# Performance work log

Hardware: AMD Instinct MI355X
Metric: run time of the kernel (lower is better)

## Reference

```python
import jax, jax.numpy as jnp
import numpy as np

D_MODEL = 1024
NUM_HEADS = 16
HEAD_DIM = D_MODEL // NUM_HEADS
SCALE = HEAD_DIM ** -0.5
BATCH = 4096
N_MODULES = 8


def setup_inputs() -> dict:
    key = jax.random.key(0)
    ks = jax.random.split(key, 7)
    s = 1.0 / np.sqrt(D_MODEL)
    return {
        "query": jax.random.normal(ks[0], (BATCH, D_MODEL), jnp.float32),
        "kv_stack": jax.random.normal(ks[1], (N_MODULES, BATCH, D_MODEL), jnp.float32),
        "Wq": jax.random.normal(ks[2], (D_MODEL, D_MODEL), jnp.float32) * s,
        "Wk": jax.random.normal(ks[3], (D_MODEL, D_MODEL), jnp.float32) * s,
        "Wv": jax.random.normal(ks[4], (D_MODEL, D_MODEL), jnp.float32) * s,
        "Wo": jax.random.normal(ks[5], (D_MODEL, D_MODEL), jnp.float32) * s,
        "bo": jnp.zeros((D_MODEL,), jnp.float32),
    }


def reference(query, kv_stack, Wq, Wk, Wv, Wo, bo):
    # query: [B, D]; kv_stack: [M, B, D] (stacked module representations)
    B = query.shape[0]
    M = kv_stack.shape[0]
    # projections (nn.Linear: x @ W.T), split into heads; seq_len == 1
    q = (query @ Wq.T).reshape(B, NUM_HEADS, HEAD_DIM)            # [B,H,hd]
    k = jnp.einsum("mbd,ed->mbe", kv_stack, Wk).reshape(M, B, NUM_HEADS, HEAD_DIM)
    v = jnp.einsum("mbd,ed->mbe", kv_stack, Wv).reshape(M, B, NUM_HEADS, HEAD_DIM)
    # scores over the single kv position: [M,B,H,1]
    scores = jnp.einsum("bhd,mbhd->mbh", q, k)[..., None] * SCALE
    attn_weights = jax.nn.softmax(scores, axis=-1)  # softmax over size-1 axis -> ones
    attn_output = attn_weights * v                   # [M,B,H,hd] (dropout is eval/no-op)
    attn_output = attn_output.reshape(M, B, D_MODEL)
    out = jnp.einsum("mbe,oe->mbo", attn_output, Wo) + bo + query  # residual per module
    return out  # [M, B, D] (stacked in kv order instead of the dict)
```

## Files before the change

kernel.cpp:

```cpp
#include <hip/hip_runtime.h>
#include <hip/hip_bf16.h>


typedef __attribute__((ext_vector_type(4))) float f32x4;
typedef __attribute__((ext_vector_type(8))) short short8;

#define D_MODEL 1024
#define BATCH   4096
#define M_ROWS  32768

__device__ __forceinline__ short f2bf(float f) {
    union { float f; unsigned u; } x; x.f = f;
    unsigned r = (x.u + 0x7fffu + ((x.u >> 16) & 1u)) >> 16;
    return (short)r;
}

__device__ __forceinline__ unsigned bfpk(float lo, float hi) {
    __hip_bfloat162 h = __float22bfloat162_rn(make_float2(lo, hi));
    unsigned u; __builtin_memcpy(&u, &h, 4); return u;
}

__device__ __forceinline__ short8 cvt8(float4 a, float4 b) {
    union { unsigned u[4]; short8 s; } r;
    r.u[0] = bfpk(a.x, a.y);
    r.u[1] = bfpk(a.z, a.w);
    r.u[2] = bfpk(b.x, b.y);
    r.u[3] = bfpk(b.z, b.w);
    return r.s;
}

__global__ __launch_bounds__(256) void fuse_w_kernel(
        const float* __restrict__ Wo, const float* __restrict__ Wv,
        short* __restrict__ Cw) {
    __shared__ __align__(16) short Ash[64][32];
    __shared__ __align__(16) short Bsh[64][32];
    const int t = threadIdx.x;
    const int lane = t & 63;
    const int w = t >> 6;
    const int wr = w >> 1, wc = w & 1;
    const int brow = blockIdx.y * 64;
    const int bcol = blockIdx.x * 64;

    f32x4 acc[2][2];
#pragma unroll
    for (int m = 0; m < 2; ++m)
#pragma unroll
        for (int n = 0; n < 2; ++n) acc[m][n] = (f32x4)(0.0f);

    for (int kt = 0; kt < 32; ++kt) {
        const float* ga = Wo + (size_t)(brow + (t >> 2)) * D_MODEL + kt * 32 + (t & 3) * 8;
        float4 a0 = *(const float4*)ga;
        float4 a1 = *(const float4*)(ga + 4);
        float4 bv[2];
#pragma unroll
        for (int j = 0; j < 2; ++j) {
            int lin = j * 256 + t;
            int e = lin >> 4, c4 = lin & 15;
            bv[j] = *(const float4*)(Wv + (size_t)(kt * 32 + e) * D_MODEL + bcol + c4 * 4);
        }
        *reinterpret_cast<short8*>(&Ash[t >> 2][(t & 3) * 8]) = cvt8(a0, a1);
#pragma unroll
        for (int j = 0; j < 2; ++j) {
            int lin = j * 256 + t;
            int e = lin >> 4, c4 = lin & 15;
            int d = c4 * 4;
            Bsh[d + 0][e] = f2bf(bv[j].x);
            Bsh[d + 1][e] = f2bf(bv[j].y);
            Bsh[d + 2][e] = f2bf(bv[j].z);
            Bsh[d + 3][e] = f2bf(bv[j].w);
        }
        __syncthreads();
        {
            const int r = lane & 15, q = lane >> 4;
            short8 af[2], bfr[2];
#pragma unroll
            for (int m = 0; m < 2; ++m)
                af[m] = *reinterpret_cast<const short8*>(&Ash[wr * 32 + m * 16 + r][q * 8]);
#pragma unroll
            for (int n = 0; n < 2; ++n)
                bfr[n] = *reinterpret_cast<const short8*>(&Bsh[wc * 32 + n * 16 + r][q * 8]);
#pragma unroll
            for (int m = 0; m < 2; ++m)
#pragma unroll
                for (int n = 0; n < 2; ++n)
                    acc[m][n] = __builtin_amdgcn_mfma_f32_16x16x32_bf16(
                        af[m], bfr[n], acc[m][n], 0, 0, 0);
        }
        __syncthreads();
    }

    const int r = lane & 15, q = lane >> 4;
#pragma unroll
    for (int m = 0; m < 2; ++m)
#pragma unroll
        for (int n = 0; n < 2; ++n)
#pragma unroll
            for (int j = 0; j < 4; ++j) {
                int o = brow + wr * 32 + m * 16 + q * 4 + j;
                int d = bcol + wc * 32 + n * 16 + r;
                Cw[(size_t)o * D_MODEL + d] = f2bf(acc[m][n][j]);
            }
}

struct AV { float4 v[2][2]; };

__global__ __launch_bounds__(256) void attn_gemm_kernel(
        const float* __restrict__ kv, const float* __restrict__ query,
        const short* __restrict__ Cw, const float* __restrict__ bo,
        float* __restrict__ out) {
    __shared__ __align__(16) short Ash[2][128][32];
    __shared__ __align__(16) short Bsh[2][128][32];
    const int t = threadIdx.x;
    const int lane = t & 63;
    const int w = t >> 6;
    const int wr = w >> 1, wc = w & 1;

    const int L = blockIdx.x;
    const int x = L & 7, j5 = L >> 3;
    const int bx = j5 & 7;
    const int rt = (j5 >> 3) * 8 + x;
    const int brow = rt * 128;

    f32x4 acc[4][4];
#pragma unroll
    for (int m = 0; m < 4; ++m)
#pragma unroll
        for (int n = 0; n < 4; ++n) acc[m][n] = (f32x4)(0.0f);

    auto load_a = [&](int kt) {
        AV a;
#pragma unroll
        for (int j = 0; j < 2; ++j) {
            const float* g = kv + (size_t)(brow + j * 64 + (t >> 2)) * D_MODEL
                             + kt * 32 + (t & 3) * 8;
            a.v[j][0] = *(const float4*)g;
            a.v[j][1] = *(const float4*)(g + 4);
        }
        return a;
    };
    auto stage_b = [&](int kt, int buf) {
#pragma unroll
        for (int i = 0; i < 2; ++i) {
            const short* g = Cw + (size_t)(bx * 128 + i * 64 + (t >> 2)) * D_MODEL
                             + kt * 32 + (t & 3) * 8;
            __builtin_amdgcn_global_load_lds(
                (const __attribute__((address_space(1))) void*)g,
                (__attribute__((address_space(3))) void*)
                    ((char*)&Bsh[buf][0][0] + i * 4096 + w * 1024),
                16, 0, 0);
        }
    };
    auto write_a = [&](int buf, const AV& a) {
#pragma unroll
        for (int j = 0; j < 2; ++j)
            *reinterpret_cast<short8*>(&Ash[buf][j * 64 + (t >> 2)][(t & 3) * 8]) =
                cvt8(a.v[j][0], a.v[j][1]);
    };
    auto compute = [&](int buf) {
        const int r = lane & 15, q = lane >> 4;
        short8 af[4], bfr[4];
#pragma unroll
        for (int m = 0; m < 4; ++m)
            af[m] = *reinterpret_cast<const short8*>(&Ash[buf][wr * 64 + m * 16 + r][q * 8]);
#pragma unroll
        for (int n = 0; n < 4; ++n)
            bfr[n] = *reinterpret_cast<const short8*>(&Bsh[buf][wc * 64 + n * 16 + r][q * 8]);
#pragma unroll
        for (int m = 0; m < 4; ++m)
#pragma unroll
            for (int n = 0; n < 4; ++n)
                acc[m][n] = __builtin_amdgcn_mfma_f32_16x16x32_bf16(
                    af[m], bfr[n], acc[m][n], 0, 0, 0);
    };

    AV a = load_a(0);
    stage_b(0, 0);
    write_a(0, a);
    __syncthreads();

#pragma unroll 2
    for (int kt = 0; kt < 32; ++kt) {
        const int cur = kt & 1;
        if (kt < 31) {
            a = load_a(kt + 1);
            stage_b(kt + 1, cur ^ 1);
        }
        compute(cur);
        if (kt < 31) write_a(cur ^ 1, a);
        __syncthreads();
    }

    const int r = lane & 15, q = lane >> 4;
#pragma unroll
    for (int n = 0; n < 4; ++n) {
        int o = bx * 128 + wc * 64 + n * 16 + r;
        float bov = bo[o];
#pragma unroll
        for (int m = 0; m < 4; ++m) {
            int gb = brow + wr * 64 + m * 16 + q * 4;
#pragma unroll
            for (int j = 0; j < 4; ++j) {
                int grow = gb + j;
                out[(size_t)grow * D_MODEL + o] =
                    acc[m][n][j] + bov +
                    query[(size_t)(grow & (BATCH - 1)) * D_MODEL + o];
            }
        }
    }
}

extern "C" void kernel_launch(void* const* d_in, const int* in_sizes, int n_in,
                              void* d_out, int out_size, void* d_ws, size_t ws_size,
                              hipStream_t stream) {
    int kv_i = 1, q_i = 0, bo_i = 6;
    int w_i[4] = {2, 3, 4, 5};
    int nw = 0;
    for (int i = 0; i < n_in; ++i) {
        long s = in_sizes[i];
        if (s == 33554432) kv_i = i;
        else if (s == 4194304) q_i = i;
        else if (s == 1024) bo_i = i;
        else if (s == 1048576 && nw < 4) w_i[nw++] = i;
    }
    const float* query = (const float*)d_in[q_i];
    const float* kv    = (const float*)d_in[kv_i];
    const float* Wv    = (const float*)d_in[w_i[2]];
    const float* Wo    = (const float*)d_in[w_i[3]];
    const float* bo    = (const float*)d_in[bo_i];
    short* Cw  = (short*)d_ws;
    float* out = (float*)d_out;

    fuse_w_kernel<<<dim3(16, 16), dim3(256), 0, stream>>>(Wo, Wv, Cw);
    attn_gemm_kernel<<<dim3(2048), dim3(256), 0, stream>>>(kv, query, Cw, bo, out);
}
```

Before: 212.3 us.

## Load MFMA operands directly from global memory, dropping LDS staging

The main GEMM kernel no longer stages A and B tiles through double-buffered shared memory. Each lane now loads its MFMA fragments straight from global memory, converting fp32 activations to bf16 in registers, which removes the LDS traffic and the per-iteration barriers. The cost is that operands shared across waves are fetched redundantly through the caches (about 2x global/L2 traffic), and there is no explicit prefetch to hide load latency behind the MFMAs.

Measured after the change: 395.7 us. +86.4%, slower.

```diff
diff --git a/kernel.cpp b/kernel.cpp
--- a/kernel.cpp
+++ b/kernel.cpp
@@ -102,18 +102,15 @@
             }
 }
 
-struct AV { float4 v[2][2]; };
-
 __global__ __launch_bounds__(256) void attn_gemm_kernel(
         const float* __restrict__ kv, const float* __restrict__ query,
         const short* __restrict__ Cw, const float* __restrict__ bo,
         float* __restrict__ out) {
-    __shared__ __align__(16) short Ash[2][128][32];
-    __shared__ __align__(16) short Bsh[2][128][32];
     const int t = threadIdx.x;
     const int lane = t & 63;
     const int w = t >> 6;
     const int wr = w >> 1, wc = w & 1;
+    const int r = lane & 15, q = lane >> 4;
 
     const int L = blockIdx.x;
     const int x = L & 7, j5 = L >> 3;
@@ -127,70 +124,35 @@
 #pragma unroll
         for (int n = 0; n < 4; ++n) acc[m][n] = (f32x4)(0.0f);
 
-    auto load_a = [&](int kt) {
-        AV a;
+    const float* aptr[4];
 #pragma unroll
-        for (int j = 0; j < 2; ++j) {
-            const float* g = kv + (size_t)(brow + j * 64 + (t >> 2)) * D_MODEL
-                             + kt * 32 + (t & 3) * 8;
-            a.v[j][0] = *(const float4*)g;
-            a.v[j][1] = *(const float4*)(g + 4);
-        }
-        return a;
-    };
-    auto stage_b = [&](int kt, int buf) {
+    for (int m = 0; m < 4; ++m)
+        aptr[m] = kv + (size_t)(brow + wr * 64 + m * 16 + r) * D_MODEL + q * 8;
+    const short* bptr[4];
 #pragma unroll
-        for (int i = 0; i < 2; ++i) {
-            const short* g = Cw + (size_t)(bx * 128 + i * 64 + (t >> 2)) * D_MODEL
-                             + kt * 32 + (t & 3) * 8;
-            __builtin_amdgcn_global_load_lds(
-                (const __attribute__((address_space(1))) void*)g,
-                (__attribute__((address_space(3))) void*)
-                    ((char*)&Bsh[buf][0][0] + i * 4096 + w * 1024),
-                16, 0, 0);
-        }
-    };
-    auto write_a = [&](int buf, const AV& a) {
-#pragma unroll
-        for (int j = 0; j < 2; ++j)
-            *reinterpret_cast<short8*>(&Ash[buf][j * 64 + (t >> 2)][(t & 3) * 8]) =
-                cvt8(a.v[j][0], a.v[j][1]);
-    };
-    auto compute = [&](int buf) {
-        const int r = lane & 15, q = lane >> 4;
+    for (int n = 0; n < 4; ++n)
+        bptr[n] = Cw + (size_t)(bx * 128 + wc * 64 + n * 16 + r) * D_MODEL + q * 8;
+
+#pragma unroll 2
+    for (int kt = 0; kt < 32; ++kt) {
         short8 af[4], bfr[4];
 #pragma unroll
-        for (int m = 0; m < 4; ++m)
-            af[m] = *reinterpret_cast<const short8*>(&Ash[buf][wr * 64 + m * 16 + r][q * 8]);
+        for (int m = 0; m < 4; ++m) {
+            float4 lo = *(const float4*)(aptr[m] + kt * 32);
+            float4 hi = *(const float4*)(aptr[m] + kt * 32 + 4);
+            af[m] = cvt8(lo, hi);
+        }
 #pragma unroll
         for (int n = 0; n < 4; ++n)
-            bfr[n] = *reinterpret_cast<const short8*>(&Bsh[buf][wc * 64 + n * 16 + r][q * 8]);
+            bfr[n] = *reinterpret_cast<const short8*>(bptr[n] + kt * 32);
 #pragma unroll
         for (int m = 0; m < 4; ++m)
 #pragma unroll
             for (int n = 0; n < 4; ++n)
                 acc[m][n] = __builtin_amdgcn_mfma_f32_16x16x32_bf16(
                     af[m], bfr[n], acc[m][n], 0, 0, 0);
-    };
-
-    AV a = load_a(0);
-    stage_b(0, 0);
-    write_a(0, a);
-    __syncthreads();
-
-#pragma unroll 2
-    for (int kt = 0; kt < 32; ++kt) {
-        const int cur = kt & 1;
-        if (kt < 31) {
-            a = load_a(kt + 1);
-            stage_b(kt + 1, cur ^ 1);
-        }
-        compute(cur);
-        if (kt < 31) write_a(cur ^ 1, a);
-        __syncthreads();
     }
 
-    const int r = lane & 15, q = lane >> 4;
 #pragma unroll
     for (int n = 0; n < 4; ++n) {
         int o = bx * 128 + wc * 64 + n * 16 + r;
```
